# Kernel optimization log

Measured on AMD Instinct MI355X. Metric: run time of the kernel, lower is better.

## Reference

```python
import jax, jax.numpy as jnp
import numpy as np

INPUT_DIM, D_MODEL, DEPTH = 64, 256, 2
B, S = 4, 4096
RES_SCALE = 0.1


def setup_inputs() -> dict:
    key = jax.random.key(0)
    ks = jax.random.split(key, 8)
    w = 0.02  # weight init scale to keep unnormalized QK^T V numerically tame
    x = jax.random.normal(ks[0], (B, S, INPUT_DIM), dtype=jnp.float32)
    W_embed = jax.random.normal(ks[1], (INPUT_DIM, D_MODEL), dtype=jnp.float32) * w
    b_embed = jnp.zeros((D_MODEL,), dtype=jnp.float32)
    Wq = jax.random.normal(ks[2], (DEPTH, D_MODEL, D_MODEL), dtype=jnp.float32) * w
    Wk = jax.random.normal(ks[3], (DEPTH, D_MODEL, D_MODEL), dtype=jnp.float32) * w
    Wv = jax.random.normal(ks[4], (DEPTH, D_MODEL, D_MODEL), dtype=jnp.float32) * w
    W_out = jax.random.normal(ks[5], (D_MODEL, 1), dtype=jnp.float32) * w
    b_out = jnp.zeros((1,), dtype=jnp.float32)
    return {"x": x, "W_embed": W_embed, "b_embed": b_embed,
            "Wq": Wq, "Wk": Wk, "Wv": Wv, "W_out": W_out, "b_out": b_out}


def reference(x, W_embed, b_embed, Wq, Wk, Wv, W_out, b_out):
    # embed: [B,S,input_dim] -> [B,S,d]
    h = x @ W_embed + b_embed
    depth = Wq.shape[0]
    for i in range(depth):  # small fixed layer loop
        Q = h @ Wq[i]
        K = h @ Wk[i]
        V = h @ Wv[i]
        # unnormalized attention: (Q K^T) V, no softmax — same matmul order as torch
        scores = jnp.einsum('bsd,btd->bst', Q, K)          # [B,S,S]
        h = h + RES_SCALE * jnp.einsum('bst,btd->bsd', scores, V)
    h = h.sum(axis=1)  # [B,d]
    return h @ W_out + b_out  # [B,1]
```

## Files before the change

### kernel.cpp

```cpp
#include <hip/hip_runtime.h>

namespace {

constexpr int BATCH = 4, SEQ = 4096, DM = 256, DP = 80, NCH = 16;
constexpr float ALPHA = 0.1f;

__device__ __forceinline__ float dot4(float4 a, float4 b) {
  return a.x * b.x + a.y * b.y + a.z * b.z + a.w * b.w;
}
__device__ __forceinline__ float dot5f4(const float* __restrict__ r,
                                        const float* v) {
  const float4* R = reinterpret_cast<const float4*>(r);
  const float4* V = reinterpret_cast<const float4*>(v);
  return ((dot4(R[0], V[0]) + dot4(R[1], V[1])) +
          (dot4(R[2], V[2]) + dot4(R[3], V[3]))) + dot4(R[4], V[4]);
}
__device__ __forceinline__ float dot10f4(const float* __restrict__ r,
                                         const float* v) {
  const float4* R = reinterpret_cast<const float4*>(r);
  const float4* V = reinterpret_cast<const float4*>(v);
  float a0 = 0.f, a1 = 0.f;
#pragma unroll
  for (int q = 0; q < 10; q += 2) {
    a0 += dot4(R[q], V[q]); a1 += dot4(R[q + 1], V[q + 1]);
  }
  return a0 + a1;
}
__device__ __forceinline__ float dot16f4(const float4* __restrict__ R,
                                         const float4* V) {
  float a0 = 0.f, a1 = 0.f, a2 = 0.f, a3 = 0.f;
#pragma unroll
  for (int q = 0; q < 16; q += 4) {
    a0 += dot4(R[q + 0], V[q + 0]); a1 += dot4(R[q + 1], V[q + 1]);
    a2 += dot4(R[q + 2], V[q + 2]); a3 += dot4(R[q + 3], V[q + 3]);
  }
  return (a0 + a1) + (a2 + a3);
}
__device__ __forceinline__ float dot32f4(const float* __restrict__ r,
                                         const float* v) {
  const float4* R = reinterpret_cast<const float4*>(r);
  const float4* V = reinterpret_cast<const float4*>(v);
  return dot16f4(R, V) + dot16f4(R + 16, V + 16);
}
__device__ __forceinline__ float dot64f4(const float* __restrict__ r,
                                         const float* v) {
  const float4* R = reinterpret_cast<const float4*>(r);
  const float4* V = reinterpret_cast<const float4*>(v);
  float a0 = 0.f, a1 = 0.f, a2 = 0.f, a3 = 0.f;
#pragma unroll 16
  for (int q = 0; q < 64; q += 4) {
    a0 += dot4(R[q + 0], V[q + 0]); a1 += dot4(R[q + 1], V[q + 1]);
    a2 += dot4(R[q + 2], V[q + 2]); a3 += dot4(R[q + 3], V[q + 3]);
  }
  return (a0 + a1) + (a2 + a3);
}
__device__ __forceinline__ float wave_red(float s) {
  s += __shfl_down(s, 32); s += __shfl_down(s, 16); s += __shfl_down(s, 8);
  s += __shfl_down(s, 4);  s += __shfl_down(s, 2);  s += __shfl_down(s, 1);
  return s;
}

__global__ __launch_bounds__(256, 2)
void k_pre(const float* __restrict__ x, const float* __restrict__ Wemb,
           const float* __restrict__ bemb, const float* __restrict__ Wq,
           const float* __restrict__ Wk, const float* __restrict__ Wv,
           const float* __restrict__ Wout,
           float* __restrict__ Xp, float* __restrict__ cp,
           float* __restrict__ F0r, float* __restrict__ P0r,
           float* __restrict__ K0r, float* __restrict__ P1r,
           float* __restrict__ K1r, float* __restrict__ PF1r,
           float* __restrict__ KF1r, float* __restrict__ w1g,
           float* __restrict__ eog) {
  const int bid = blockIdx.x, t = threadIdx.x;
  __shared__ __align__(16) float esT[512];
  __shared__ __align__(16) float fsT[512];
  __shared__ __align__(16) float psT[512];
  __shared__ __align__(16) float4 ppA[4][64];
  __shared__ __align__(16) float4 ppB[4][64];
  __shared__ __align__(16) float xs[2][16][64];
  __shared__ __align__(16) float cs[16][64];
  __shared__ __align__(16) float vbuf[256];

  if (bid < 231) {
    const int role = bid / 33, grp = bid % 33;
    const int r0 = grp * 2, nr = (r0 == 64) ? 1 : 2;
    {
      const float v0 = (r0 < 64) ? Wemb[(size_t)r0 * DM + t] : bemb[t];
      float v1 = 0.f;
      if (nr == 2) v1 = (r0 + 1 < 64) ? Wemb[(size_t)(r0 + 1) * DM + t] : bemb[t];
      esT[t * 2] = v0; esT[t * 2 + 1] = v1;
    }
    __syncthreads();
    const int jg = t & 63, ks = t >> 6, j0 = jg * 4;

    auto nt_pass = [&](const float* src, const float* __restrict__ M,
                       float* dstT, float* dstR) {
      float4 A0 = make_float4(0.f, 0.f, 0.f, 0.f);
      float4 A1 = make_float4(0.f, 0.f, 0.f, 0.f);
      const float* Mp = M + (size_t)(ks * 64) * DM + j0;
#pragma unroll 16
      for (int i = 0; i < 64; ++i) {
        const float4 m = *reinterpret_cast<const float4*>(Mp + (size_t)i * DM);
        const float s0 = src[(ks * 64 + i) * 2];
        const float s1 = src[(ks * 64 + i) * 2 + 1];
        A0.x += s0 * m.x; A0.y += s0 * m.y; A0.z += s0 * m.z; A0.w += s0 * m.w;
        A1.x += s1 * m.x; A1.y += s1 * m.y; A1.z += s1 * m.z; A1.w += s1 * m.w;
      }
      ppA[ks][jg] = A0; ppB[ks][jg] = A1;
      __syncthreads();
      if (t < 128) {
        const int rr = t >> 6, jj = t & 63;
        float4 q0, q1, q2, q3;
        if (rr == 0) { q0 = ppA[0][jj]; q1 = ppA[1][jj]; q2 = ppA[2][jj]; q3 = ppA[3][jj]; }
        else         { q0 = ppB[0][jj]; q1 = ppB[1][jj]; q2 = ppB[2][jj]; q3 = ppB[3][jj]; }
        const float4 s = make_float4((q0.x + q1.x) + (q2.x + q3.x),
                                     (q0.y + q1.y) + (q2.y + q3.y),
                                     (q0.z + q1.z) + (q2.z + q3.z),
                                     (q0.w + q1.w) + (q2.w + q3.w));
        if (dstT) {
          dstT[(jj * 4 + 0) * 2 + rr] = s.x;
          dstT[(jj * 4 + 1) * 2 + rr] = s.y;
          dstT[(jj * 4 + 2) * 2 + rr] = s.z;
          dstT[(jj * 4 + 3) * 2 + rr] = s.w;
        }
        if (dstR && rr < nr)
          *reinterpret_cast<float4*>(&dstR[(size_t)(r0 + rr) * DM + jj * 4]) = s;
      }
      __syncthreads();
    };

    const float* Wq1 = Wq + (size_t)DM * DM;
    const float* Wk1 = Wk + (size_t)DM * DM;
    float* dstR;
    if (role == 0)      { dstR = F0r;  nt_pass(esT, Wv,  nullptr, dstR); }
    else if (role == 1) { dstR = P0r;  nt_pass(esT, Wq,  nullptr, dstR); }
    else if (role == 2) { dstR = K0r;  nt_pass(esT, Wk,  nullptr, dstR); }
    else if (role == 3) { dstR = P1r;  nt_pass(esT, Wq1, nullptr, dstR); }
    else if (role == 4) { dstR = K1r;  nt_pass(esT, Wk1, nullptr, dstR); }
    else if (role == 5) {
      dstR = PF1r;
      nt_pass(esT, Wv, fsT, nullptr);
      nt_pass(fsT, Wq1, nullptr, dstR);
    } else {
      dstR = KF1r;
      nt_pass(esT, Wv, fsT, nullptr);
      nt_pass(fsT, Wk1, nullptr, dstR);
    }
    if (grp == 32) {
      for (int rr = 65; rr < DP; ++rr) dstR[(size_t)rr * DM + t] = 0.f;
    }
  } else if (bid < 359) {
    const int idx = bid - 231;
    const int per_b = NCH * 2;
    const int b = idx / per_b, r5 = idx % per_b, ch = r5 >> 1, half = r5 & 1;
    const int chrows = SEQ / NCH, nstage = chrows / 16;
    const float* xb = x + ((size_t)b * SEQ + (size_t)ch * chrows) * 64;
    const int trs = t >> 4, tcs = t & 15;
    const int tr2 = t >> 3, tc2 = t & 7;

    float acc[2][4] = {{0.f, 0.f, 0.f, 0.f}, {0.f, 0.f, 0.f, 0.f}};
    float4 csum = make_float4(0.f, 0.f, 0.f, 0.f);
    float4 v = *reinterpret_cast<const float4*>(xb + (size_t)trs * 64 + tcs * 4);
    int buf = 0;
    for (int st = 0; st < nstage; ++st) {
      *reinterpret_cast<float4*>(&xs[buf][trs][tcs * 4]) = v;
      csum.x += v.x; csum.y += v.y; csum.z += v.z; csum.w += v.w;
      __syncthreads();
      float4 vn = make_float4(0.f, 0.f, 0.f, 0.f);
      if (st + 1 < nstage)
        vn = *reinterpret_cast<const float4*>(
            xb + (size_t)((st + 1) * 16 + trs) * 64 + tcs * 4);
#pragma unroll
      for (int s = 0; s < 16; ++s) {
        const float a0 = xs[buf][s][tr2 * 2 + 0];
        const float a1 = xs[buf][s][tr2 * 2 + 1];
        const float4 b4 =
            *reinterpret_cast<const float4*>(&xs[buf][s][half * 32 + tc2 * 4]);
        acc[0][0] += a0 * b4.x; acc[0][1] += a0 * b4.y;
        acc[0][2] += a0 * b4.z; acc[0][3] += a0 * b4.w;
        acc[1][0] += a1 * b4.x; acc[1][1] += a1 * b4.y;
        acc[1][2] += a1 * b4.z; acc[1][3] += a1 * b4.w;
      }
      v = vn; buf ^= 1;
    }
    float* Xpb = Xp + (size_t)(b * NCH + ch) * 4096;
#pragma unroll
    for (int rr = 0; rr < 2; ++rr) {
      const float4 s4 = make_float4(acc[rr][0], acc[rr][1], acc[rr][2], acc[rr][3]);
      *reinterpret_cast<float4*>(
          &Xpb[(size_t)(tr2 * 2 + rr) * 64 + half * 32 + tc2 * 4]) = s4;
    }
    if (half == 0) {
      *reinterpret_cast<float4*>(&cs[trs][tcs * 4]) = csum;
      __syncthreads();
      if (t < 64) {
        float s = 0.f;
#pragma unroll
        for (int g = 0; g < 16; ++g) s += cs[g][t];
        cp[(size_t)(b * NCH + ch) * 64 + t] = s;
      }
    }
  } else if (bid == 359) {
    vbuf[t] = Wout[t];
    __syncthreads();
    if (t < 160) {
      const int i = t >> 1, s = t & 1;
      const float* row = (i < 64) ? Wemb + (size_t)i * DM : (i == 64) ? bemb : nullptr;
      float a = row ? dot32f4(row + s * 128, vbuf + s * 128) : 0.f;
      a += __shfl_down(a, 1);
      if (s == 0) eog[i] = a;
    }
  } else {
    vbuf[t] = Wout[t];
    __syncthreads();
    const float* Wv1 = Wv + (size_t)DM * DM;
    w1g[t] = dot64f4(Wv1 + (size_t)t * DM, vbuf);
  }
}

__global__ __launch_bounds__(256, 2)
void k_mid(const float* __restrict__ Wemb, const float* __restrict__ bemb,
           const float* __restrict__ Wout,
           const float* __restrict__ F0r, const float* __restrict__ P0r,
           const float* __restrict__ K0r, const float* __restrict__ P1r,
           const float* __restrict__ K1r, const float* __restrict__ PF1r,
           const float* __restrict__ KF1r, const float* __restrict__ w1g,
           float* __restrict__ C0, float* __restrict__ C0T,
           float* __restrict__ C1, float* __restrict__ CY,
           float* __restrict__ D1, float* __restrict__ DY,
           float* __restrict__ e1g, float* __restrict__ f1g,
           float* __restrict__ f0g) {
  const int bid = blockIdx.x, t = threadIdx.x;
  __shared__ __align__(16) float bvs[256];
  if (bid < 400) {
    const int mat = bid / 80, j = bid % 80;
    const float* bsrc = (mat == 0) ? K0r : (mat < 3) ? K1r : KF1r;
    bvs[t] = bsrc[(size_t)j * DM + t];
    __syncthreads();
    if (t < 160) {
      const int i = t >> 1, s = t & 1;
      const float* A = (mat == 0) ? P0r : (mat == 1 || mat == 3) ? P1r : PF1r;
      float a = dot32f4(A + (size_t)i * DM + s * 128, bvs + s * 128);
      a += __shfl_down(a, 1);
      if (s == 0) {
        if (mat == 0) { C0[j * DP + i] = a; C0T[i * DP + j] = a; }
        else if (mat == 1) C1[j * DP + i] = a;
        else if (mat == 2) CY[j * DP + i] = a;
        else if (mat == 3) D1[j * DP + i] = a;
        else DY[j * DP + i] = a;
      }
    }
  } else {
    const int which = bid - 400;
    bvs[t] = (which == 2) ? Wout[t] : w1g[t];
    __syncthreads();
    if (t < 160) {
      const int i = t >> 1, s = t & 1;
      const float* row;
      if (which == 0)
        row = (i < 64) ? Wemb + (size_t)i * DM : (i == 64) ? bemb : nullptr;
      else
        row = (i < 65) ? F0r + (size_t)i * DM : nullptr;
      float a = row ? dot32f4(row + s * 128, bvs + s * 128) : 0.f;
      a += __shfl_down(a, 1);
      if (s == 0) {
        if (which == 0) e1g[i] = a;
        else if (which == 1) f1g[i] = a;
        else f0g[i] = a;
      }
    }
  }
}

__global__ __launch_bounds__(1024, 4)
void k_post(const float* __restrict__ Xp, const float* __restrict__ cp,
            const float* __restrict__ C0, const float* __restrict__ C0T,
            const float* __restrict__ C1, const float* __restrict__ CY,
            const float* __restrict__ D1, const float* __restrict__ DY,
            const float* __restrict__ eog, const float* __restrict__ f0g,
            const float* __restrict__ e1g, const float* __restrict__ f1g,
            const float* __restrict__ bout, float* __restrict__ out) {
  const int b = blockIdx.x, t = threadIdx.x;
  __shared__ __align__(16) float X[80][81];
  __shared__ __align__(16) float cl[DP], eo[DP], f0[DP], e1[DP], f1[DP];
  __shared__ __align__(16) float cM0[DP], g8[DP], y8[DP], qv[DP];
  __shared__ __align__(16) float rE[DP], rF[DP], t1v[DP], Xq[DP];
  __shared__ __align__(16) float pr0[DP], pr1[DP], pr2[DP];
  __shared__ float dots[3];

  {
    const int e = t * 4;
    const float* base = Xp + (size_t)b * NCH * 4096 + e;
    float4 a0 = make_float4(0.f, 0.f, 0.f, 0.f), a1 = a0, a2 = a0, a3 = a0;
#pragma unroll
    for (int ch = 0; ch < NCH; ch += 4) {
      const float4 p0 = *reinterpret_cast<const float4*>(base + (size_t)ch * 4096);
      const float4 p1 = *reinterpret_cast<const float4*>(base + (size_t)(ch + 1) * 4096);
      const float4 p2 = *reinterpret_cast<const float4*>(base + (size_t)(ch + 2) * 4096);
      const float4 p3 = *reinterpret_cast<const float4*>(base + (size_t)(ch + 3) * 4096);
      a0.x += p0.x; a0.y += p0.y; a0.z += p0.z; a0.w += p0.w;
      a1.x += p1.x; a1.y += p1.y; a1.z += p1.z; a1.w += p1.w;
      a2.x += p2.x; a2.y += p2.y; a2.z += p2.z; a2.w += p2.w;
      a3.x += p3.x; a3.y += p3.y; a3.z += p3.z; a3.w += p3.w;
    }
    const float4 s = make_float4((a0.x + a1.x) + (a2.x + a3.x),
                                 (a0.y + a1.y) + (a2.y + a3.y),
                                 (a0.z + a1.z) + (a2.z + a3.z),
                                 (a0.w + a1.w) + (a2.w + a3.w));
    const int r = t >> 4, c = (t & 15) * 4;
    X[r][c] = s.x; X[r][c + 1] = s.y; X[r][c + 2] = s.z; X[r][c + 3] = s.w;

    if (t < 64) {
      const float* cb = cp + (size_t)b * NCH * 64 + t;
      float v0 = 0.f, v1 = 0.f, v2 = 0.f, v3 = 0.f;
#pragma unroll
      for (int ch = 0; ch < NCH; ch += 4) {
        v0 += cb[(size_t)(ch + 0) * 64]; v1 += cb[(size_t)(ch + 1) * 64];
        v2 += cb[(size_t)(ch + 2) * 64]; v3 += cb[(size_t)(ch + 3) * 64];
      }
      cl[t] = (v0 + v1) + (v2 + v3);
    } else if (t == 64) cl[64] = (float)SEQ;
    else if (t < 80) cl[t] = 0.f;
    else if (t >= 128 && t < 208) eo[t - 128] = eog[t - 128];
    else if (t >= 208 && t < 288) f0[t - 208] = f0g[t - 208];
    else if (t >= 288 && t < 368) e1[t - 288] = e1g[t - 288];
    else if (t >= 368 && t < 448) f1[t - 368] = f1g[t - 368];
    if (t >= 448) {
      for (int n = t - 448; n < 2255; n += 576) {
        if (n < 1040) X[n >> 4][65 + (n & 15)] = 0.f;
        else { const int m = n - 1040; X[65 + m / 81][m % 81] = 0.f; }
      }
    }
  }
  __syncthreads();

  if (t < 320) {
    const int j = t >> 2, s = t & 3;
    float a = dot5f4(C0 + j * DP + s * 20, cl + s * 20);
    a += __shfl_down(a, 2); a += __shfl_down(a, 1);
    if (s == 0) cM0[j] = a;
  } else if (t >= 384 && t < 513) {
    const int n = t - 384;
    if (n < 64) X[n][64] = cl[n];
    else if (n == 64) X[64][64] = (float)SEQ;
    else X[64][n - 65] = cl[n - 65];
  } else if (t >= 576 && t < 656) {
    const int i = t - 576; pr0[i] = cl[i] * eo[i];
  }
  __syncthreads();

  if (t < 320) {
    const int j = t >> 2, s = t & 3;
    float a = 0.f;
    for (int i = s * 20; i < s * 20 + 20; ++i) a += cM0[i] * X[i][j];
    a += __shfl_down(a, 2); a += __shfl_down(a, 1);
    if (s == 0) g8[j] = a;
  } else if (t < 640) {
    const int u = t - 320, i = u >> 2, s = u & 3;
    float a = 0.f;
    for (int j = s * 20; j < s * 20 + 20; ++j) a += X[i][j] * f1[j];
    a += __shfl_down(a, 2); a += __shfl_down(a, 1);
    if (s == 0) y8[i] = a;
  }
  __syncthreads();

  if (t < 320) {
    const int j = t >> 2, s = t & 3;
    float a = (s < 2) ? dot10f4(C1 + j * DP + s * 40, cl + s * 40)
                      : ALPHA * dot10f4(CY + j * DP + (s - 2) * 40, g8 + (s - 2) * 40);
    a += __shfl_down(a, 2); a += __shfl_down(a, 1);
    if (s == 0) rE[j] = a;
  } else if (t < 640) {
    const int u = t - 320, j = u >> 2, s = u & 3;
    float a = (s < 2) ? dot10f4(D1 + j * DP + s * 40, cl + s * 40)
                      : ALPHA * dot10f4(DY + j * DP + (s - 2) * 40, g8 + (s - 2) * 40);
    a += __shfl_down(a, 2); a += __shfl_down(a, 1);
    if (s == 0) rF[j] = a;
  } else if (t < 960) {
    const int u = t - 640, j = u >> 2, s = u & 3;
    float a = dot5f4(C0T + j * DP + s * 20, y8 + s * 20);
    a += __shfl_down(a, 2); a += __shfl_down(a, 1);
    if (s == 0) qv[j] = e1[j] + ALPHA * a;
  }
  __syncthreads();

  if (t < 320) {
    const int j = t >> 2, s = t & 3;
    float a = 0.f;
    for (int i = s * 20; i < s * 20 + 20; ++i) a += rF[i] * X[i][j];
    a += __shfl_down(a, 2); a += __shfl_down(a, 1);
    if (s == 0) t1v[j] = a;
  } else if (t < 640) {
    const int u = t - 320, i = u >> 2, s = u & 3;
    float a = 0.f;
    for (int j = s * 20; j < s * 20 + 20; ++j) a += X[i][j] * qv[j];
    a += __shfl_down(a, 2); a += __shfl_down(a, 1);
    if (s == 0) Xq[i] = a;
  } else if (t < 720) {
    const int i = t - 640; pr1[i] = g8[i] * f0[i];
  }
  __syncthreads();

  if (t < 320) {
    const int j = t >> 2, s = t & 3;
    float a = dot5f4(C0T + j * DP + s * 20, t1v + s * 20);
    a += __shfl_down(a, 2); a += __shfl_down(a, 1);
    if (s == 0) pr2[j] = (rE[j] + ALPHA * a) * Xq[j];
  }
  __syncthreads();

  const int w = t >> 6, l = t & 63;
  if (w < 3) {
    const float* pr = (w == 0) ? pr0 : (w == 1) ? pr1 : pr2;
    float v = pr[l] + ((l < 16) ? pr[64 + l] : 0.f);
    v = wave_red(v);
    if (l == 0) dots[w] = v;
  }
  __syncthreads();
  if (t == 0) out[b] = dots[0] + ALPHA * dots[1] + ALPHA * dots[2] + bout[0];
}

}

extern "C" void kernel_launch(void* const* d_in, const int* in_sizes, int n_in,
                              void* d_out, int out_size, void* d_ws, size_t ws_size,
                              hipStream_t stream) {
  const float* x    = (const float*)d_in[0];
  const float* Wemb = (const float*)d_in[1];
  const float* bemb = (const float*)d_in[2];
  const float* Wq   = (const float*)d_in[3];
  const float* Wk   = (const float*)d_in[4];
  const float* Wv   = (const float*)d_in[5];
  const float* Wout = (const float*)d_in[6];
  const float* bout = (const float*)d_in[7];
  float* out = (float*)d_out;

  float* p = (float*)d_ws;
  float* Xp   = p; p += (size_t)BATCH * NCH * 4096;
  float* cp   = p; p += (size_t)BATCH * NCH * 64;
  float* F0r  = p; p += DP * 256;
  float* P0r  = p; p += DP * 256;
  float* K0r  = p; p += DP * 256;
  float* P1r  = p; p += DP * 256;
  float* K1r  = p; p += DP * 256;
  float* PF1r = p; p += DP * 256;
  float* KF1r = p; p += DP * 256;
  float* w1g  = p; p += 256;
  float* eog  = p; p += 80;
  float* e1g  = p; p += 80;
  float* f1g  = p; p += 80;
  float* f0g  = p; p += 80;
  float* C0   = p; p += DP * DP;
  float* C0T  = p; p += DP * DP;
  float* C1   = p; p += DP * DP;
  float* CY   = p; p += DP * DP;
  float* D1   = p; p += DP * DP;
  float* DY   = p; p += DP * DP;

  k_pre<<<361, 256, 0, stream>>>(x, Wemb, bemb, Wq, Wk, Wv, Wout,
                                 Xp, cp, F0r, P0r, K0r, P1r, K1r, PF1r, KF1r,
                                 w1g, eog);
  k_mid<<<403, 256, 0, stream>>>(Wemb, bemb, Wout, F0r, P0r, K0r, P1r, K1r,
                                 PF1r, KF1r, w1g, C0, C0T, C1, CY, D1, DY,
                                 e1g, f1g, f0g);
  k_post<<<BATCH, 1024, 0, stream>>>(Xp, cp, C0, C0T, C1, CY, D1, DY,
                                     eog, f0g, e1g, f1g, bout, out);
}
```

Before: 33.16 us.

## Move chunk reduction and c·M0 work from serial post kernel into parallel mid kernel

The chunk-partial reduction of Xp and cp, the construction of the padded 81-stride X matrix, and the cM0 vector (computed as K0·(P0ᵀ·cl) instead of the old C0·cl path) now run in extra blocks of the middle kernel. This takes work off the four-block final kernel, which is latency bound. The e1/f1/f0 vectors are computed directly from Wv and Wout in a single pre-kernel block, which drops the F0r role and the w1g round trip. The cost is a heavier serial pre-kernel block, extra workspace traffic for Xg, and a reassociated floating-point order.

```diff
diff --git a/kernel.cpp b/kernel.cpp
--- a/kernel.cpp
+++ b/kernel.cpp
@@ -66,22 +66,22 @@
            const float* __restrict__ Wk, const float* __restrict__ Wv,
            const float* __restrict__ Wout,
            float* __restrict__ Xp, float* __restrict__ cp,
-           float* __restrict__ F0r, float* __restrict__ P0r,
+           float* __restrict__ P0r, float* __restrict__ P0t,
            float* __restrict__ K0r, float* __restrict__ P1r,
            float* __restrict__ K1r, float* __restrict__ PF1r,
-           float* __restrict__ KF1r, float* __restrict__ w1g,
-           float* __restrict__ eog) {
+           float* __restrict__ KF1r,
+           float* __restrict__ eog, float* __restrict__ e1g,
+           float* __restrict__ f1g, float* __restrict__ f0g) {
   const int bid = blockIdx.x, t = threadIdx.x;
   __shared__ __align__(16) float esT[512];
   __shared__ __align__(16) float fsT[512];
-  __shared__ __align__(16) float psT[512];
   __shared__ __align__(16) float4 ppA[4][64];
   __shared__ __align__(16) float4 ppB[4][64];
   __shared__ __align__(16) float xs[2][16][64];
   __shared__ __align__(16) float cs[16][64];
-  __shared__ __align__(16) float vbuf[256];
-
-  if (bid < 231) {
+  __shared__ __align__(16) float vbuf[256], w1s[256], vv0s[256], vvos[256];
+
+  if (bid < 198) {
     const int role = bid / 33, grp = bid % 33;
     const int r0 = grp * 2, nr = (r0 == 64) ? 1 : 2;
     {
@@ -94,7 +94,7 @@
     const int jg = t & 63, ks = t >> 6, j0 = jg * 4;
 
     auto nt_pass = [&](const float* src, const float* __restrict__ M,
-                       float* dstT, float* dstR) {
+                       float* dstT, float* dstR, float* dstRt) {
       float4 A0 = make_float4(0.f, 0.f, 0.f, 0.f);
       float4 A1 = make_float4(0.f, 0.f, 0.f, 0.f);
       const float* Mp = M + (size_t)(ks * 64) * DM + j0;
@@ -125,6 +125,12 @@
         }
         if (dstR && rr < nr)
           *reinterpret_cast<float4*>(&dstR[(size_t)(r0 + rr) * DM + jj * 4]) = s;
+        if (dstRt && rr < nr) {
+          dstRt[(size_t)(jj * 4 + 0) * DP + r0 + rr] = s.x;
+          dstRt[(size_t)(jj * 4 + 1) * DP + r0 + rr] = s.y;
+          dstRt[(size_t)(jj * 4 + 2) * DP + r0 + rr] = s.z;
+          dstRt[(size_t)(jj * 4 + 3) * DP + r0 + rr] = s.w;
+        }
       }
       __syncthreads();
     };
@@ -132,25 +138,26 @@
     const float* Wq1 = Wq + (size_t)DM * DM;
     const float* Wk1 = Wk + (size_t)DM * DM;
     float* dstR;
-    if (role == 0)      { dstR = F0r;  nt_pass(esT, Wv,  nullptr, dstR); }
-    else if (role == 1) { dstR = P0r;  nt_pass(esT, Wq,  nullptr, dstR); }
-    else if (role == 2) { dstR = K0r;  nt_pass(esT, Wk,  nullptr, dstR); }
-    else if (role == 3) { dstR = P1r;  nt_pass(esT, Wq1, nullptr, dstR); }
-    else if (role == 4) { dstR = K1r;  nt_pass(esT, Wk1, nullptr, dstR); }
-    else if (role == 5) {
+    if (role == 0)      { dstR = P0r; nt_pass(esT, Wq,  nullptr, P0r, P0t); }
+    else if (role == 1) { dstR = K0r; nt_pass(esT, Wk,  nullptr, K0r, nullptr); }
+    else if (role == 2) { dstR = P1r; nt_pass(esT, Wq1, nullptr, P1r, nullptr); }
+    else if (role == 3) { dstR = K1r; nt_pass(esT, Wk1, nullptr, K1r, nullptr); }
+    else if (role == 4) {
       dstR = PF1r;
-      nt_pass(esT, Wv, fsT, nullptr);
-      nt_pass(fsT, Wq1, nullptr, dstR);
+      nt_pass(esT, Wv, fsT, nullptr, nullptr);
+      nt_pass(fsT, Wq1, nullptr, PF1r, nullptr);
     } else {
       dstR = KF1r;
-      nt_pass(esT, Wv, fsT, nullptr);
-      nt_pass(fsT, Wk1, nullptr, dstR);
+      nt_pass(esT, Wv, fsT, nullptr, nullptr);
+      nt_pass(fsT, Wk1, nullptr, KF1r, nullptr);
     }
     if (grp == 32) {
       for (int rr = 65; rr < DP; ++rr) dstR[(size_t)rr * DM + t] = 0.f;
-    }
-  } else if (bid < 359) {
-    const int idx = bid - 231;
+      if (role == 0)
+        for (int i = 65; i < DP; ++i) P0t[(size_t)t * DP + i] = 0.f;
+    }
+  } else if (bid < 326) {
+    const int idx = bid - 198;
     const int per_b = NCH * 2;
     const int b = idx / per_b, r5 = idx % per_b, ch = r5 >> 1, half = r5 & 1;
     const int chrows = SEQ / NCH, nstage = chrows / 16;
@@ -200,38 +207,50 @@
         cp[(size_t)(b * NCH + ch) * 64 + t] = s;
       }
     }
-  } else if (bid == 359) {
+  } else {
     vbuf[t] = Wout[t];
+    __syncthreads();
+    const float* Wv0 = Wv;
+    const float* Wv1 = Wv + (size_t)DM * DM;
+    w1s[t]  = dot64f4(Wv1 + (size_t)t * DM, vbuf);
+    vvos[t] = dot64f4(Wv0 + (size_t)t * DM, vbuf);
+    __syncthreads();
+    vv0s[t] = dot64f4(Wv0 + (size_t)t * DM, w1s);
     __syncthreads();
     if (t < 160) {
       const int i = t >> 1, s = t & 1;
-      const float* row = (i < 64) ? Wemb + (size_t)i * DM : (i == 64) ? bemb : nullptr;
-      float a = row ? dot32f4(row + s * 128, vbuf + s * 128) : 0.f;
-      a += __shfl_down(a, 1);
-      if (s == 0) eog[i] = a;
-    }
-  } else {
-    vbuf[t] = Wout[t];
-    __syncthreads();
-    const float* Wv1 = Wv + (size_t)DM * DM;
-    w1g[t] = dot64f4(Wv1 + (size_t)t * DM, vbuf);
+      const float* row = (i < 64) ? Wemb + (size_t)i * DM
+                                  : (i == 64) ? bemb : nullptr;
+      float aeo = 0.f, ae1 = 0.f, af1 = 0.f, af0 = 0.f;
+      if (row) {
+        aeo = dot32f4(row + s * 128, vbuf + s * 128);
+        ae1 = dot32f4(row + s * 128, w1s + s * 128);
+        af1 = dot32f4(row + s * 128, vv0s + s * 128);
+        af0 = dot32f4(row + s * 128, vvos + s * 128);
+      }
+      aeo += __shfl_down(aeo, 1); ae1 += __shfl_down(ae1, 1);
+      af1 += __shfl_down(af1, 1); af0 += __shfl_down(af0, 1);
+      if (s == 0) { eog[i] = aeo; e1g[i] = ae1; f1g[i] = af1; f0g[i] = af0; }
+    }
   }
 }
 
 __global__ __launch_bounds__(256, 2)
-void k_mid(const float* __restrict__ Wemb, const float* __restrict__ bemb,
-           const float* __restrict__ Wout,
-           const float* __restrict__ F0r, const float* __restrict__ P0r,
+void k_mid(const float* __restrict__ Xp, const float* __restrict__ cp,
+           const float* __restrict__ P0r, const float* __restrict__ P0t,
            const float* __restrict__ K0r, const float* __restrict__ P1r,
            const float* __restrict__ K1r, const float* __restrict__ PF1r,
-           const float* __restrict__ KF1r, const float* __restrict__ w1g,
-           float* __restrict__ C0, float* __restrict__ C0T,
-           float* __restrict__ C1, float* __restrict__ CY,
-           float* __restrict__ D1, float* __restrict__ DY,
-           float* __restrict__ e1g, float* __restrict__ f1g,
-           float* __restrict__ f0g) {
+           const float* __restrict__ KF1r, const float* __restrict__ eog,
+           float* __restrict__ C0T, float* __restrict__ C1,
+           float* __restrict__ CY, float* __restrict__ D1,
+           float* __restrict__ DY, float* __restrict__ Xg,
+           float* __restrict__ clg, float* __restrict__ cM0g,
+           float* __restrict__ dot0g) {
   const int bid = blockIdx.x, t = threadIdx.x;
   __shared__ __align__(16) float bvs[256];
+  __shared__ __align__(16) float clS[DP], eoS[DP];
+  __shared__ __align__(16) float vP0[256];
+
   if (bid < 400) {
     const int mat = bid / 80, j = bid % 80;
     const float* bsrc = (mat == 0) ? K0r : (mat < 3) ? K1r : KF1r;
@@ -243,109 +262,98 @@
       float a = dot32f4(A + (size_t)i * DM + s * 128, bvs + s * 128);
       a += __shfl_down(a, 1);
       if (s == 0) {
-        if (mat == 0) { C0[j * DP + i] = a; C0T[i * DP + j] = a; }
+        if (mat == 0) C0T[i * DP + j] = a;
         else if (mat == 1) C1[j * DP + i] = a;
         else if (mat == 2) CY[j * DP + i] = a;
         else if (mat == 3) D1[j * DP + i] = a;
         else DY[j * DP + i] = a;
       }
     }
+  } else if (bid < 464) {
+    const int idx = bid - 400;
+    const int b = idx >> 4, sl = idx & 15;
+    const int e = sl * 256 + t;
+    const float* base = Xp + (size_t)b * NCH * 4096 + e;
+    float a0 = 0.f, a1 = 0.f, a2 = 0.f, a3 = 0.f;
+#pragma unroll
+    for (int ch = 0; ch < NCH; ch += 4) {
+      a0 += base[(size_t)(ch + 0) * 4096]; a1 += base[(size_t)(ch + 1) * 4096];
+      a2 += base[(size_t)(ch + 2) * 4096]; a3 += base[(size_t)(ch + 3) * 4096];
+    }
+    Xg[(size_t)b * 6480 + (e >> 6) * 81 + (e & 63)] = (a0 + a1) + (a2 + a3);
   } else {
-    const int which = bid - 400;
-    bvs[t] = (which == 2) ? Wout[t] : w1g[t];
+    const int b = bid - 464;
+    if (t < 64) {
+      const float* cb = cp + (size_t)b * NCH * 64 + t;
+      float v0 = 0.f, v1 = 0.f, v2 = 0.f, v3 = 0.f;
+#pragma unroll
+      for (int ch = 0; ch < NCH; ch += 4) {
+        v0 += cb[(size_t)(ch + 0) * 64]; v1 += cb[(size_t)(ch + 1) * 64];
+        v2 += cb[(size_t)(ch + 2) * 64]; v3 += cb[(size_t)(ch + 3) * 64];
+      }
+      clS[t] = (v0 + v1) + (v2 + v3);
+    } else if (t == 64) clS[64] = (float)SEQ;
+    else if (t < 80) clS[t] = 0.f;
+    else if (t >= 128 && t < 208) eoS[t - 128] = eog[t - 128];
+    __syncthreads();
+    vP0[t] = dot10f4(P0t + (size_t)t * DP, clS) +
+             dot10f4(P0t + (size_t)t * DP + 40, clS + 40);
     __syncthreads();
     if (t < 160) {
-      const int i = t >> 1, s = t & 1;
-      const float* row;
-      if (which == 0)
-        row = (i < 64) ? Wemb + (size_t)i * DM : (i == 64) ? bemb : nullptr;
-      else
-        row = (i < 65) ? F0r + (size_t)i * DM : nullptr;
-      float a = row ? dot32f4(row + s * 128, bvs + s * 128) : 0.f;
+      const int j = t >> 1, s = t & 1;
+      float a = dot32f4(K0r + (size_t)j * DM + s * 128, vP0 + s * 128);
       a += __shfl_down(a, 1);
-      if (s == 0) {
-        if (which == 0) e1g[i] = a;
-        else if (which == 1) f1g[i] = a;
-        else f0g[i] = a;
-      }
-    }
+      if (s == 0) cM0g[b * DP + j] = a;
+    } else if (t >= 192) {
+      const int l = t - 192;
+      float v = clS[l] * eoS[l] + ((l < 16) ? clS[64 + l] * eoS[64 + l] : 0.f);
+      v = wave_red(v);
+      if (l == 0) dot0g[b] = v;
+    }
+    float* XB = Xg + (size_t)b * 6480;
+    for (int n = t; n < 2384; n += 256) {
+      if (n < 64) XB[n * 81 + 64] = clS[n];
+      else if (n < 128) XB[64 * 81 + (n - 64)] = clS[n - 64];
+      else if (n == 128) XB[64 * 81 + 64] = (float)SEQ;
+      else if (n < 1169) {
+        const int m = n - 129;
+        XB[(m >> 4) * 81 + 65 + (m & 15)] = 0.f;
+      } else {
+        const int m = n - 1169;
+        XB[(65 + m / 81) * 81 + m % 81] = 0.f;
+      }
+    }
+    if (t < 80) clg[b * DP + t] = clS[t];
   }
 }
 
 __global__ __launch_bounds__(1024, 4)
-void k_post(const float* __restrict__ Xp, const float* __restrict__ cp,
-            const float* __restrict__ C0, const float* __restrict__ C0T,
-            const float* __restrict__ C1, const float* __restrict__ CY,
-            const float* __restrict__ D1, const float* __restrict__ DY,
-            const float* __restrict__ eog, const float* __restrict__ f0g,
-            const float* __restrict__ e1g, const float* __restrict__ f1g,
+void k_post(const float* __restrict__ Xg, const float* __restrict__ clg,
+            const float* __restrict__ cM0g, const float* __restrict__ dot0g,
+            const float* __restrict__ C0T, const float* __restrict__ C1,
+            const float* __restrict__ CY, const float* __restrict__ D1,
+            const float* __restrict__ DY, const float* __restrict__ e1g,
+            const float* __restrict__ f1g, const float* __restrict__ f0g,
             const float* __restrict__ bout, float* __restrict__ out) {
   const int b = blockIdx.x, t = threadIdx.x;
   __shared__ __align__(16) float X[80][81];
-  __shared__ __align__(16) float cl[DP], eo[DP], f0[DP], e1[DP], f1[DP];
-  __shared__ __align__(16) float cM0[DP], g8[DP], y8[DP], qv[DP];
+  __shared__ __align__(16) float cl[DP], cM0[DP], e1[DP], f1[DP], f0[DP];
+  __shared__ __align__(16) float g8[DP], y8[DP], qv[DP];
   __shared__ __align__(16) float rE[DP], rF[DP], t1v[DP], Xq[DP];
-  __shared__ __align__(16) float pr0[DP], pr1[DP], pr2[DP];
-  __shared__ float dots[3];
+  __shared__ __align__(16) float pr1[DP], pr2[DP];
+  __shared__ float dots[2], d0s;
 
   {
-    const int e = t * 4;
-    const float* base = Xp + (size_t)b * NCH * 4096 + e;
-    float4 a0 = make_float4(0.f, 0.f, 0.f, 0.f), a1 = a0, a2 = a0, a3 = a0;
-#pragma unroll
-    for (int ch = 0; ch < NCH; ch += 4) {
-      const float4 p0 = *reinterpret_cast<const float4*>(base + (size_t)ch * 4096);
-      const float4 p1 = *reinterpret_cast<const float4*>(base + (size_t)(ch + 1) * 4096);
-      const float4 p2 = *reinterpret_cast<const float4*>(base + (size_t)(ch + 2) * 4096);
-      const float4 p3 = *reinterpret_cast<const float4*>(base + (size_t)(ch + 3) * 4096);
-      a0.x += p0.x; a0.y += p0.y; a0.z += p0.z; a0.w += p0.w;
-      a1.x += p1.x; a1.y += p1.y; a1.z += p1.z; a1.w += p1.w;
-      a2.x += p2.x; a2.y += p2.y; a2.z += p2.z; a2.w += p2.w;
-      a3.x += p3.x; a3.y += p3.y; a3.z += p3.z; a3.w += p3.w;
-    }
-    const float4 s = make_float4((a0.x + a1.x) + (a2.x + a3.x),
-                                 (a0.y + a1.y) + (a2.y + a3.y),
-                                 (a0.z + a1.z) + (a2.z + a3.z),
-                                 (a0.w + a1.w) + (a2.w + a3.w));
-    const int r = t >> 4, c = (t & 15) * 4;
-    X[r][c] = s.x; X[r][c + 1] = s.y; X[r][c + 2] = s.z; X[r][c + 3] = s.w;
-
-    if (t < 64) {
-      const float* cb = cp + (size_t)b * NCH * 64 + t;
-      float v0 = 0.f, v1 = 0.f, v2 = 0.f, v3 = 0.f;
-#pragma unroll
-      for (int ch = 0; ch < NCH; ch += 4) {
-        v0 += cb[(size_t)(ch + 0) * 64]; v1 += cb[(size_t)(ch + 1) * 64];
-        v2 += cb[(size_t)(ch + 2) * 64]; v3 += cb[(size_t)(ch + 3) * 64];
-      }
-      cl[t] = (v0 + v1) + (v2 + v3);
-    } else if (t == 64) cl[64] = (float)SEQ;
-    else if (t < 80) cl[t] = 0.f;
-    else if (t >= 128 && t < 208) eo[t - 128] = eog[t - 128];
-    else if (t >= 208 && t < 288) f0[t - 208] = f0g[t - 208];
-    else if (t >= 288 && t < 368) e1[t - 288] = e1g[t - 288];
-    else if (t >= 368 && t < 448) f1[t - 368] = f1g[t - 368];
-    if (t >= 448) {
-      for (int n = t - 448; n < 2255; n += 576) {
-        if (n < 1040) X[n >> 4][65 + (n & 15)] = 0.f;
-        else { const int m = n - 1040; X[65 + m / 81][m % 81] = 0.f; }
-      }
-    }
-  }
-  __syncthreads();
-
-  if (t < 320) {
-    const int j = t >> 2, s = t & 3;
-    float a = dot5f4(C0 + j * DP + s * 20, cl + s * 20);
-    a += __shfl_down(a, 2); a += __shfl_down(a, 1);
-    if (s == 0) cM0[j] = a;
-  } else if (t >= 384 && t < 513) {
-    const int n = t - 384;
-    if (n < 64) X[n][64] = cl[n];
-    else if (n == 64) X[64][64] = (float)SEQ;
-    else X[64][n - 65] = cl[n - 65];
-  } else if (t >= 576 && t < 656) {
-    const int i = t - 576; pr0[i] = cl[i] * eo[i];
+    float* Xf = &X[0][0];
+    const float4* src = reinterpret_cast<const float4*>(Xg + (size_t)b * 6480);
+    float4* dst = reinterpret_cast<float4*>(Xf);
+    for (int n = t; n < 1620; n += 1024) dst[n] = src[n];
+    if (t < 80) cl[t] = clg[b * DP + t];
+    else if (t < 160) cM0[t - 80] = cM0g[b * DP + t - 80];
+    else if (t < 240) e1[t - 160] = e1g[t - 160];
+    else if (t < 320) f1[t - 240] = f1g[t - 240];
+    else if (t < 400) f0[t - 320] = f0g[t - 320];
+    else if (t == 1023) d0s = dot0g[b];
   }
   __syncthreads();
 
@@ -410,14 +418,14 @@
   __syncthreads();
 
   const int w = t >> 6, l = t & 63;
-  if (w < 3) {
-    const float* pr = (w == 0) ? pr0 : (w == 1) ? pr1 : pr2;
+  if (w < 2) {
+    const float* pr = (w == 0) ? pr1 : pr2;
     float v = pr[l] + ((l < 16) ? pr[64 + l] : 0.f);
     v = wave_red(v);
     if (l == 0) dots[w] = v;
   }
   __syncthreads();
-  if (t == 0) out[b] = dots[0] + ALPHA * dots[1] + ALPHA * dots[2] + bout[0];
+  if (t == 0) out[b] = d0s + ALPHA * dots[0] + ALPHA * dots[1] + bout[0];
 }
 
 }
@@ -438,31 +446,32 @@
   float* p = (float*)d_ws;
   float* Xp   = p; p += (size_t)BATCH * NCH * 4096;
   float* cp   = p; p += (size_t)BATCH * NCH * 64;
-  float* F0r  = p; p += DP * 256;
   float* P0r  = p; p += DP * 256;
+  float* P0t  = p; p += 256 * DP;
   float* K0r  = p; p += DP * 256;
   float* P1r  = p; p += DP * 256;
   float* K1r  = p; p += DP * 256;
   float* PF1r = p; p += DP * 256;
   float* KF1r = p; p += DP * 256;
-  float* w1g  = p; p += 256;
-  float* eog  = p; p += 80;
-  float* e1g  = p; p += 80;
-  float* f1g  = p; p += 80;
-  float* f0g  = p; p += 80;
-  float* C0   = p; p += DP * DP;
+  float* eog  = p; p += DP;
+  float* e1g  = p; p += DP;
+  float* f1g  = p; p += DP;
+  float* f0g  = p; p += DP;
   float* C0T  = p; p += DP * DP;
   float* C1   = p; p += DP * DP;
   float* CY   = p; p += DP * DP;
   float* D1   = p; p += DP * DP;
   float* DY   = p; p += DP * DP;
-
-  k_pre<<<361, 256, 0, stream>>>(x, Wemb, bemb, Wq, Wk, Wv, Wout,
-                                 Xp, cp, F0r, P0r, K0r, P1r, K1r, PF1r, KF1r,
-                                 w1g, eog);
-  k_mid<<<403, 256, 0, stream>>>(Wemb, bemb, Wout, F0r, P0r, K0r, P1r, K1r,
-                                 PF1r, KF1r, w1g, C0, C0T, C1, CY, D1, DY,
-                                 e1g, f1g, f0g);
-  k_post<<<BATCH, 1024, 0, stream>>>(Xp, cp, C0, C0T, C1, CY, D1, DY,
-                                     eog, f0g, e1g, f1g, bout, out);
-}
+  float* Xg   = p; p += (size_t)BATCH * 6480;
+  float* clg  = p; p += BATCH * DP;
+  float* cM0g = p; p += BATCH * DP;
+  float* dot0g = p; p += BATCH;
+
+  k_pre<<<327, 256, 0, stream>>>(x, Wemb, bemb, Wq, Wk, Wv, Wout,
+                                 Xp, cp, P0r, P0t, K0r, P1r, K1r, PF1r, KF1r,
+                                 eog, e1g, f1g, f0g);
+  k_mid<<<468, 256, 0, stream>>>(Xp, cp, P0r, P0t, K0r, P1r, K1r, PF1r, KF1r,
+                                 eog, C0T, C1, CY, D1, DY, Xg, clg, cM0g, dot0g);
+  k_post<<<BATCH, 1024, 0, stream>>>(Xg, clg, cM0g, dot0g, C0T, C1, CY, D1, DY,
+                                     e1g, f1g, f0g, bout, out);
+}
```

After: 60.82 us. 1.83x slower.

## Eliminate k_mid by applying low-rank factors directly as matrix-vector products in k_post

Applied to the files above, without the earlier changes.

Drops the middle kernel that formed the 80x80 products C0, C1, CY, D1 and DY from the 80x256 factors. k_post instead applies each factor pair as two chained matrix-vector products, and computes e1, f1 and f0 inline. This removes a kernel launch and the global round trip of the intermediate matrices. In exchange, the 4-block post kernel does more serial matvec stages with extra barriers and strided column reads of the factor matrices.

```diff
diff --git a/kernel.cpp b/kernel.cpp
--- a/kernel.cpp
+++ b/kernel.cpp
@@ -7,24 +7,6 @@
 
 __device__ __forceinline__ float dot4(float4 a, float4 b) {
   return a.x * b.x + a.y * b.y + a.z * b.z + a.w * b.w;
-}
-__device__ __forceinline__ float dot5f4(const float* __restrict__ r,
-                                        const float* v) {
-  const float4* R = reinterpret_cast<const float4*>(r);
-  const float4* V = reinterpret_cast<const float4*>(v);
-  return ((dot4(R[0], V[0]) + dot4(R[1], V[1])) +
-          (dot4(R[2], V[2]) + dot4(R[3], V[3]))) + dot4(R[4], V[4]);
-}
-__device__ __forceinline__ float dot10f4(const float* __restrict__ r,
-                                         const float* v) {
-  const float4* R = reinterpret_cast<const float4*>(r);
-  const float4* V = reinterpret_cast<const float4*>(v);
-  float a0 = 0.f, a1 = 0.f;
-#pragma unroll
-  for (int q = 0; q < 10; q += 2) {
-    a0 += dot4(R[q], V[q]); a1 += dot4(R[q + 1], V[q + 1]);
-  }
-  return a0 + a1;
 }
 __device__ __forceinline__ float dot16f4(const float4* __restrict__ R,
                                          const float4* V) {
@@ -35,6 +17,18 @@
     a2 += dot4(R[q + 2], V[q + 2]); a3 += dot4(R[q + 3], V[q + 3]);
   }
   return (a0 + a1) + (a2 + a3);
+}
+__device__ __forceinline__ void dot16f4_2(const float4* __restrict__ R,
+                                          const float4* V1, const float4* V2,
+                                          float& o1, float& o2) {
+  float a0 = 0.f, a1 = 0.f, b0 = 0.f, b1 = 0.f;
+#pragma unroll
+  for (int q = 0; q < 16; q += 2) {
+    const float4 m0 = R[q], m1 = R[q + 1];
+    a0 += dot4(m0, V1[q]); a1 += dot4(m1, V1[q + 1]);
+    b0 += dot4(m0, V2[q]); b1 += dot4(m1, V2[q + 1]);
+  }
+  o1 = a0 + a1; o2 = b0 + b1;
 }
 __device__ __forceinline__ float dot32f4(const float* __restrict__ r,
                                          const float* v) {
@@ -58,6 +52,19 @@
   s += __shfl_down(s, 32); s += __shfl_down(s, 16); s += __shfl_down(s, 8);
   s += __shfl_down(s, 4);  s += __shfl_down(s, 2);  s += __shfl_down(s, 1);
   return s;
+}
+__device__ __forceinline__ float colacc(const float* __restrict__ M,
+                                        const float* v, int k, int i0, int cnt) {
+  float a0 = 0.f, a1 = 0.f, a2 = 0.f, a3 = 0.f;
+  const float* p = M + (size_t)i0 * DM + k;
+#pragma unroll 4
+  for (int i = 0; i < cnt; i += 4) {
+    a0 += v[i0 + i + 0] * p[(size_t)(i + 0) * DM];
+    a1 += v[i0 + i + 1] * p[(size_t)(i + 1) * DM];
+    a2 += v[i0 + i + 2] * p[(size_t)(i + 2) * DM];
+    a3 += v[i0 + i + 3] * p[(size_t)(i + 3) * DM];
+  }
+  return (a0 + a1) + (a2 + a3);
 }
 
 __global__ __launch_bounds__(256, 2)
@@ -74,7 +81,6 @@
   const int bid = blockIdx.x, t = threadIdx.x;
   __shared__ __align__(16) float esT[512];
   __shared__ __align__(16) float fsT[512];
-  __shared__ __align__(16) float psT[512];
   __shared__ __align__(16) float4 ppA[4][64];
   __shared__ __align__(16) float4 ppB[4][64];
   __shared__ __align__(16) float xs[2][16][64];
@@ -218,167 +224,170 @@
   }
 }
 
-__global__ __launch_bounds__(256, 2)
-void k_mid(const float* __restrict__ Wemb, const float* __restrict__ bemb,
-           const float* __restrict__ Wout,
-           const float* __restrict__ F0r, const float* __restrict__ P0r,
-           const float* __restrict__ K0r, const float* __restrict__ P1r,
-           const float* __restrict__ K1r, const float* __restrict__ PF1r,
-           const float* __restrict__ KF1r, const float* __restrict__ w1g,
-           float* __restrict__ C0, float* __restrict__ C0T,
-           float* __restrict__ C1, float* __restrict__ CY,
-           float* __restrict__ D1, float* __restrict__ DY,
-           float* __restrict__ e1g, float* __restrict__ f1g,
-           float* __restrict__ f0g) {
-  const int bid = blockIdx.x, t = threadIdx.x;
-  __shared__ __align__(16) float bvs[256];
-  if (bid < 400) {
-    const int mat = bid / 80, j = bid % 80;
-    const float* bsrc = (mat == 0) ? K0r : (mat < 3) ? K1r : KF1r;
-    bvs[t] = bsrc[(size_t)j * DM + t];
-    __syncthreads();
-    if (t < 160) {
-      const int i = t >> 1, s = t & 1;
-      const float* A = (mat == 0) ? P0r : (mat == 1 || mat == 3) ? P1r : PF1r;
-      float a = dot32f4(A + (size_t)i * DM + s * 128, bvs + s * 128);
-      a += __shfl_down(a, 1);
-      if (s == 0) {
-        if (mat == 0) { C0[j * DP + i] = a; C0T[i * DP + j] = a; }
-        else if (mat == 1) C1[j * DP + i] = a;
-        else if (mat == 2) CY[j * DP + i] = a;
-        else if (mat == 3) D1[j * DP + i] = a;
-        else DY[j * DP + i] = a;
-      }
-    }
-  } else {
-    const int which = bid - 400;
-    bvs[t] = (which == 2) ? Wout[t] : w1g[t];
-    __syncthreads();
-    if (t < 160) {
-      const int i = t >> 1, s = t & 1;
-      const float* row;
-      if (which == 0)
-        row = (i < 64) ? Wemb + (size_t)i * DM : (i == 64) ? bemb : nullptr;
-      else
-        row = (i < 65) ? F0r + (size_t)i * DM : nullptr;
-      float a = row ? dot32f4(row + s * 128, bvs + s * 128) : 0.f;
-      a += __shfl_down(a, 1);
-      if (s == 0) {
-        if (which == 0) e1g[i] = a;
-        else if (which == 1) f1g[i] = a;
-        else f0g[i] = a;
-      }
-    }
-  }
-}
-
 __global__ __launch_bounds__(1024, 4)
 void k_post(const float* __restrict__ Xp, const float* __restrict__ cp,
-            const float* __restrict__ C0, const float* __restrict__ C0T,
-            const float* __restrict__ C1, const float* __restrict__ CY,
-            const float* __restrict__ D1, const float* __restrict__ DY,
-            const float* __restrict__ eog, const float* __restrict__ f0g,
-            const float* __restrict__ e1g, const float* __restrict__ f1g,
-            const float* __restrict__ bout, float* __restrict__ out) {
+            const float* __restrict__ Wemb, const float* __restrict__ bemb,
+            const float* __restrict__ Wout,
+            const float* __restrict__ F0r, const float* __restrict__ P0r,
+            const float* __restrict__ K0r, const float* __restrict__ P1r,
+            const float* __restrict__ K1r, const float* __restrict__ PF1r,
+            const float* __restrict__ KF1r, const float* __restrict__ w1g,
+            const float* __restrict__ eog, const float* __restrict__ bout,
+            float* __restrict__ out) {
   const int b = blockIdx.x, t = threadIdx.x;
-  __shared__ __align__(16) float X[80][81];
-  __shared__ __align__(16) float cl[DP], eo[DP], f0[DP], e1[DP], f1[DP];
+  __shared__ __align__(16) float X[80][84];
+  __shared__ __align__(16) float vA[256], vP1[256], vF[256], vB[256], vC[256];
+  __shared__ __align__(16) float w1l[256], wol[256];
+  __shared__ __align__(16) float cl[DP], eo[DP], e1[DP], f1[DP], f0[DP];
   __shared__ __align__(16) float cM0[DP], g8[DP], y8[DP], qv[DP];
   __shared__ __align__(16) float rE[DP], rF[DP], t1v[DP], Xq[DP];
-  __shared__ __align__(16) float pr0[DP], pr1[DP], pr2[DP];
-  __shared__ float dots[3];
+  __shared__ __align__(16) float pr1[DP], pr2[DP];
+  __shared__ float dots[2], d0s;
+
+  if (t < 512) {
+    const int e = t * 8;
+    const float* base = Xp + (size_t)b * NCH * 4096 + e;
+    float4 aA = make_float4(0.f, 0.f, 0.f, 0.f), aB = aA;
+#pragma unroll 4
+    for (int ch = 0; ch < NCH; ++ch) {
+      const float4 p1 = *reinterpret_cast<const float4*>(base + (size_t)ch * 4096);
+      const float4 p2 = *reinterpret_cast<const float4*>(base + (size_t)ch * 4096 + 4);
+      aA.x += p1.x; aA.y += p1.y; aA.z += p1.z; aA.w += p1.w;
+      aB.x += p2.x; aB.y += p2.y; aB.z += p2.z; aB.w += p2.w;
+    }
+    const int r = t >> 3, c = (t & 7) * 8;
+    *reinterpret_cast<float4*>(&X[r][c]) = aA;
+    *reinterpret_cast<float4*>(&X[r][c + 4]) = aB;
+  } else if (t < 576) {
+    const int i = t - 512;
+    const float* cb = cp + (size_t)b * NCH * 64 + i;
+    float v0 = 0.f, v1 = 0.f, v2 = 0.f, v3 = 0.f;
+#pragma unroll
+    for (int ch = 0; ch < NCH; ch += 4) {
+      v0 += cb[(size_t)(ch + 0) * 64]; v1 += cb[(size_t)(ch + 1) * 64];
+      v2 += cb[(size_t)(ch + 2) * 64]; v3 += cb[(size_t)(ch + 3) * 64];
+    }
+    cl[i] = (v0 + v1) + (v2 + v3);
+    if (i == 0) cl[64] = (float)SEQ;
+    if (i == 1) for (int p = 65; p < DP; ++p) cl[p] = 0.f;
+  } else if (t < 640) {
+    reinterpret_cast<float4*>(w1l)[t - 576] =
+        reinterpret_cast<const float4*>(w1g)[t - 576];
+  } else if (t < 704) {
+    reinterpret_cast<float4*>(wol)[t - 640] =
+        reinterpret_cast<const float4*>(Wout)[t - 640];
+  } else if (t < 784) {
+    eo[t - 704] = eog[t - 704];
+  } else {
+    for (int m = t - 784; m < 2160; m += 240) {
+      if (m < 960) X[m / 15][65 + m % 15] = 0.f;
+      else { const int q = m - 960; X[65 + q / 80][q % 80] = 0.f; }
+    }
+  }
+  __syncthreads();
+
+  if (t < 320) {
+    const int i = t >> 2, s = t & 3;
+    const float* row = (i < 64) ? Wemb + (size_t)i * DM : (i == 64) ? bemb : nullptr;
+    float a = row ? dot16f4(reinterpret_cast<const float4*>(row + s * 64),
+                            reinterpret_cast<const float4*>(w1l + s * 64)) : 0.f;
+    a += __shfl_down(a, 2); a += __shfl_down(a, 1);
+    if (s == 0) e1[i] = a;
+  } else if (t < 640) {
+    const int u = t - 320, i = u >> 2, s = u & 3;
+    float a = dot16f4(reinterpret_cast<const float4*>(F0r + (size_t)i * DM + s * 64),
+                      reinterpret_cast<const float4*>(w1l + s * 64));
+    a += __shfl_down(a, 2); a += __shfl_down(a, 1);
+    if (s == 0) f1[i] = a;
+  } else if (t < 960) {
+    const int u = t - 640, i = u >> 2, s = u & 3;
+    float a = dot16f4(reinterpret_cast<const float4*>(F0r + (size_t)i * DM + s * 64),
+                      reinterpret_cast<const float4*>(wol + s * 64));
+    a += __shfl_down(a, 2); a += __shfl_down(a, 1);
+    if (s == 0) f0[i] = a;
+  } else {
+    for (int m = t - 960; m < 129; m += 64) {
+      if (m < 64) X[m][64] = cl[m];
+      else if (m < 128) X[64][m - 64] = cl[m - 64];
+      else X[64][64] = (float)SEQ;
+    }
+  }
+  __syncthreads();
 
   {
-    const int e = t * 4;
-    const float* base = Xp + (size_t)b * NCH * 4096 + e;
-    float4 a0 = make_float4(0.f, 0.f, 0.f, 0.f), a1 = a0, a2 = a0, a3 = a0;
-#pragma unroll
-    for (int ch = 0; ch < NCH; ch += 4) {
-      const float4 p0 = *reinterpret_cast<const float4*>(base + (size_t)ch * 4096);
-      const float4 p1 = *reinterpret_cast<const float4*>(base + (size_t)(ch + 1) * 4096);
-      const float4 p2 = *reinterpret_cast<const float4*>(base + (size_t)(ch + 2) * 4096);
-      const float4 p3 = *reinterpret_cast<const float4*>(base + (size_t)(ch + 3) * 4096);
-      a0.x += p0.x; a0.y += p0.y; a0.z += p0.z; a0.w += p0.w;
-      a1.x += p1.x; a1.y += p1.y; a1.z += p1.z; a1.w += p1.w;
-      a2.x += p2.x; a2.y += p2.y; a2.z += p2.z; a2.w += p2.w;
-      a3.x += p3.x; a3.y += p3.y; a3.z += p3.z; a3.w += p3.w;
-    }
-    const float4 s = make_float4((a0.x + a1.x) + (a2.x + a3.x),
-                                 (a0.y + a1.y) + (a2.y + a3.y),
-                                 (a0.z + a1.z) + (a2.z + a3.z),
-                                 (a0.w + a1.w) + (a2.w + a3.w));
-    const int r = t >> 4, c = (t & 15) * 4;
-    X[r][c] = s.x; X[r][c + 1] = s.y; X[r][c + 2] = s.z; X[r][c + 3] = s.w;
-
-    if (t < 64) {
-      const float* cb = cp + (size_t)b * NCH * 64 + t;
-      float v0 = 0.f, v1 = 0.f, v2 = 0.f, v3 = 0.f;
-#pragma unroll
-      for (int ch = 0; ch < NCH; ch += 4) {
-        v0 += cb[(size_t)(ch + 0) * 64]; v1 += cb[(size_t)(ch + 1) * 64];
-        v2 += cb[(size_t)(ch + 2) * 64]; v3 += cb[(size_t)(ch + 3) * 64];
-      }
-      cl[t] = (v0 + v1) + (v2 + v3);
-    } else if (t == 64) cl[64] = (float)SEQ;
-    else if (t < 80) cl[t] = 0.f;
-    else if (t >= 128 && t < 208) eo[t - 128] = eog[t - 128];
-    else if (t >= 208 && t < 288) f0[t - 208] = f0g[t - 208];
-    else if (t >= 288 && t < 368) e1[t - 288] = e1g[t - 288];
-    else if (t >= 368 && t < 448) f1[t - 368] = f1g[t - 368];
-    if (t >= 448) {
-      for (int n = t - 448; n < 2255; n += 576) {
-        if (n < 1040) X[n >> 4][65 + (n & 15)] = 0.f;
-        else { const int m = n - 1040; X[65 + m / 81][m % 81] = 0.f; }
-      }
-    }
+    const int u = (t < 512) ? t : t - 512;
+    const int k = u >> 1, s = u & 1;
+    const float* M = (t < 512) ? P0r : P1r;
+    float a = colacc(M, cl, k, s * 40, 40);
+    a += __shfl_down(a, 1);
+    if (s == 0) { if (t < 512) vA[k] = a; else vP1[k] = a; }
   }
   __syncthreads();
 
   if (t < 320) {
     const int j = t >> 2, s = t & 3;
-    float a = dot5f4(C0 + j * DP + s * 20, cl + s * 20);
+    float a = dot16f4(reinterpret_cast<const float4*>(K0r + (size_t)j * DM + s * 64),
+                      reinterpret_cast<const float4*>(vA + s * 64));
     a += __shfl_down(a, 2); a += __shfl_down(a, 1);
     if (s == 0) cM0[j] = a;
-  } else if (t >= 384 && t < 513) {
-    const int n = t - 384;
-    if (n < 64) X[n][64] = cl[n];
-    else if (n == 64) X[64][64] = (float)SEQ;
-    else X[64][n - 65] = cl[n - 65];
-  } else if (t >= 576 && t < 656) {
-    const int i = t - 576; pr0[i] = cl[i] * eo[i];
-  }
-  __syncthreads();
-
-  if (t < 320) {
-    const int j = t >> 2, s = t & 3;
-    float a = 0.f;
-    for (int i = s * 20; i < s * 20 + 20; ++i) a += cM0[i] * X[i][j];
-    a += __shfl_down(a, 2); a += __shfl_down(a, 1);
-    if (s == 0) g8[j] = a;
   } else if (t < 640) {
     const int u = t - 320, i = u >> 2, s = u & 3;
     float a = 0.f;
     for (int j = s * 20; j < s * 20 + 20; ++j) a += X[i][j] * f1[j];
     a += __shfl_down(a, 2); a += __shfl_down(a, 1);
     if (s == 0) y8[i] = a;
+  } else if (t < 704) {
+    const int l = t - 640;
+    float v = cl[l] * eo[l] + ((l < 16) ? cl[64 + l] * eo[64 + l] : 0.f);
+    v = wave_red(v);
+    if (l == 0) d0s = v;
   }
   __syncthreads();
 
   if (t < 320) {
     const int j = t >> 2, s = t & 3;
-    float a = (s < 2) ? dot10f4(C1 + j * DP + s * 40, cl + s * 40)
-                      : ALPHA * dot10f4(CY + j * DP + (s - 2) * 40, g8 + (s - 2) * 40);
+    float a = 0.f;
+    for (int i = s * 20; i < s * 20 + 20; ++i) a += cM0[i] * X[i][j];
+    a += __shfl_down(a, 2); a += __shfl_down(a, 1);
+    if (s == 0) g8[j] = a;
+  } else if (t < 832) {
+    const int u = t - 320, k = u >> 1, s = u & 1;
+    float a = colacc(K0r, y8, k, s * 40, 40);
+    a += __shfl_down(a, 1);
+    if (s == 0) vB[k] = a;
+  }
+  __syncthreads();
+
+  {
+    const int k = t >> 2, s = t & 3;
+    float a = colacc(PF1r, g8, k, s * 20, 20);
+    a += __shfl_down(a, 2); a += __shfl_down(a, 1);
+    if (s == 0) vF[k] = a;
+  }
+  __syncthreads();
+
+  if (t < 320) {
+    const int j = t >> 2, s = t & 3;
+    float a1, a2;
+    dot16f4_2(reinterpret_cast<const float4*>(K1r + (size_t)j * DM + s * 64),
+              reinterpret_cast<const float4*>(vP1 + s * 64),
+              reinterpret_cast<const float4*>(vF + s * 64), a1, a2);
+    float a = a1 + ALPHA * a2;
     a += __shfl_down(a, 2); a += __shfl_down(a, 1);
     if (s == 0) rE[j] = a;
   } else if (t < 640) {
     const int u = t - 320, j = u >> 2, s = u & 3;
-    float a = (s < 2) ? dot10f4(D1 + j * DP + s * 40, cl + s * 40)
-                      : ALPHA * dot10f4(DY + j * DP + (s - 2) * 40, g8 + (s - 2) * 40);
+    float a1, a2;
+    dot16f4_2(reinterpret_cast<const float4*>(KF1r + (size_t)j * DM + s * 64),
+              reinterpret_cast<const float4*>(vP1 + s * 64),
+              reinterpret_cast<const float4*>(vF + s * 64), a1, a2);
+    float a = a1 + ALPHA * a2;
     a += __shfl_down(a, 2); a += __shfl_down(a, 1);
     if (s == 0) rF[j] = a;
   } else if (t < 960) {
     const int u = t - 640, j = u >> 2, s = u & 3;
-    float a = dot5f4(C0T + j * DP + s * 20, y8 + s * 20);
+    float a = dot16f4(reinterpret_cast<const float4*>(P0r + (size_t)j * DM + s * 64),
+                      reinterpret_cast<const float4*>(vB + s * 64));
     a += __shfl_down(a, 2); a += __shfl_down(a, 1);
     if (s == 0) qv[j] = e1[j] + ALPHA * a;
   }
@@ -401,23 +410,32 @@
   }
   __syncthreads();
 
+  {
+    const int k = t >> 2, s = t & 3;
+    float a = colacc(K0r, t1v, k, s * 20, 20);
+    a += __shfl_down(a, 2); a += __shfl_down(a, 1);
+    if (s == 0) vC[k] = a;
+  }
+  __syncthreads();
+
   if (t < 320) {
     const int j = t >> 2, s = t & 3;
-    float a = dot5f4(C0T + j * DP + s * 20, t1v + s * 20);
+    float a = dot16f4(reinterpret_cast<const float4*>(P0r + (size_t)j * DM + s * 64),
+                      reinterpret_cast<const float4*>(vC + s * 64));
     a += __shfl_down(a, 2); a += __shfl_down(a, 1);
     if (s == 0) pr2[j] = (rE[j] + ALPHA * a) * Xq[j];
   }
   __syncthreads();
 
   const int w = t >> 6, l = t & 63;
-  if (w < 3) {
-    const float* pr = (w == 0) ? pr0 : (w == 1) ? pr1 : pr2;
+  if (w < 2) {
+    const float* pr = (w == 0) ? pr1 : pr2;
     float v = pr[l] + ((l < 16) ? pr[64 + l] : 0.f);
     v = wave_red(v);
     if (l == 0) dots[w] = v;
   }
   __syncthreads();
-  if (t == 0) out[b] = dots[0] + ALPHA * dots[1] + ALPHA * dots[2] + bout[0];
+  if (t == 0) out[b] = d0s + ALPHA * dots[0] + ALPHA * dots[1] + bout[0];
 }
 
 }
@@ -446,23 +464,12 @@
   float* PF1r = p; p += DP * 256;
   float* KF1r = p; p += DP * 256;
   float* w1g  = p; p += 256;
-  float* eog  = p; p += 80;
-  float* e1g  = p; p += 80;
-  float* f1g  = p; p += 80;
-  float* f0g  = p; p += 80;
-  float* C0   = p; p += DP * DP;
-  float* C0T  = p; p += DP * DP;
-  float* C1   = p; p += DP * DP;
-  float* CY   = p; p += DP * DP;
-  float* D1   = p; p += DP * DP;
-  float* DY   = p; p += DP * DP;
+  float* eog  = p; p += DP;
 
   k_pre<<<361, 256, 0, stream>>>(x, Wemb, bemb, Wq, Wk, Wv, Wout,
                                  Xp, cp, F0r, P0r, K0r, P1r, K1r, PF1r, KF1r,
                                  w1g, eog);
-  k_mid<<<403, 256, 0, stream>>>(Wemb, bemb, Wout, F0r, P0r, K0r, P1r, K1r,
-                                 PF1r, KF1r, w1g, C0, C0T, C1, CY, D1, DY,
-                                 e1g, f1g, f0g);
-  k_post<<<BATCH, 1024, 0, stream>>>(Xp, cp, C0, C0T, C1, CY, D1, DY,
-                                     eog, f0g, e1g, f1g, bout, out);
-}
+  k_post<<<BATCH, 1024, 0, stream>>>(Xp, cp, Wemb, bemb, Wout,
+                                     F0r, P0r, K0r, P1r, K1r, PF1r, KF1r,
+                                     w1g, eog, bout, out);
+}
```

Result: slower. 54.49 us (+64.3%).
